# Kernel tuning notes

Hardware: AMD Instinct MI355X
Metric: run time of the kernel (lower is better)

## Reference

```python
import jax, jax.numpy as jnp
import numpy as np

B, C, H, W = 4, 256, 64, 64
C8 = C // 8


def setup_inputs() -> dict:
    key = jax.random.key(0)
    ks = jax.random.split(key, 9)
    s_in = 1.0 / np.sqrt(C)
    return {
        "x": jax.random.normal(ks[0], (B, C, H, W), dtype=jnp.float32),
        "Wq": jax.random.normal(ks[1], (C8, C), dtype=jnp.float32) * s_in,
        "bq": jax.random.normal(ks[2], (C8,), dtype=jnp.float32) * 0.01,
        "Wk": jax.random.normal(ks[3], (C8, C), dtype=jnp.float32) * s_in,
        "bk": jax.random.normal(ks[4], (C8,), dtype=jnp.float32) * 0.01,
        "Wv": jax.random.normal(ks[5], (C, C), dtype=jnp.float32) * s_in,
        "bv": jax.random.normal(ks[6], (C,), dtype=jnp.float32) * 0.01,
        "Wo": jax.random.normal(ks[7], (C, C), dtype=jnp.float32) * s_in,
        "bo": jax.random.normal(ks[8], (C,), dtype=jnp.float32) * 0.01,
    }


def reference(x, Wq, bq, Wk, bk, Wv, bv, Wo, bo):
    b, c, h, w = x.shape
    n = h * w
    xf = x.reshape(b, c, n)                                   # (B, C, N)
    # 1x1 convs are channel GEMMs
    q = jnp.einsum('bcn,dc->bnd', xf, Wq) + bq                # (B, N, C8)
    k = jnp.einsum('bcn,dc->bdn', xf, Wk) + bk[:, None]       # (B, C8, N)
    v = jnp.einsum('bcn,dc->bdn', xf, Wv) + bv[:, None]       # (B, C, N)
    energy = jnp.einsum('bnd,bdm->bnm', q, k)                 # (B, N, N)
    attn = jax.nn.softmax(energy, axis=-1)
    # out[b,c,i] = sum_j v[b,c,j] * attn[b,i,j]
    out = jnp.einsum('bcj,bij->bci', v, attn)                 # (B, C, N)
    out = out.reshape(b, c, h, w) + x                         # residual
    out = jnp.einsum('bchw,dc->bdhw', out, Wo) + bo[None, :, None, None]
    return out
```

## Files before the change

kernel.cpp:

```cpp
#include <hip/hip_runtime.h>

#define DEV __device__ __forceinline__

constexpr int B_  = 4;
constexpr int C_  = 256;
constexpr int C8_ = 32;
constexpr int N_  = 4096;
constexpr float LOG2E = 1.4426950408889634f;

using u16 = unsigned short;
using u32 = unsigned int;

typedef __attribute__((ext_vector_type(8))) short bf16x8;
typedef __attribute__((ext_vector_type(4))) float f32x4;

DEV float bf2f(u16 u) { return __uint_as_float(((u32)u) << 16); }
DEV u16   f2bf(float f) {
  u32 i = __float_as_uint(f);
  i += 0x7fffu + ((i >> 16) & 1u);
  return (u16)(i >> 16);
}
DEV u32 pack_rtz(float a, float b) {
  return __builtin_amdgcn_perm(__float_as_uint(b), __float_as_uint(a), 0x07060302);
}

DEV void lds_barrier() {
  asm volatile("s_waitcnt lgkmcnt(0)\n\ts_barrier" ::: "memory");
}

__global__ __launch_bounds__(256) void prep(
    const float* __restrict__ Wq, const float* __restrict__ Wk,
    const float* __restrict__ Wv, const float* __restrict__ Wo,
    u16* __restrict__ WqH, u16* __restrict__ WqL,
    u16* __restrict__ WkH, u16* __restrict__ WkL,
    u16* __restrict__ WvH,
    u16* __restrict__ WoH, u16* __restrict__ WoL)
{
  const int i = blockIdx.x * 256 + threadIdx.x;
  if (i < 8192) {
    float v = Wq[i] * LOG2E;
    u16 h = f2bf(v); WqH[i] = h; WqL[i] = f2bf(v - bf2f(h));
  } else if (i < 16384) {
    int off = i - 8192;
    float v = Wk[off];
    u16 h = f2bf(v); WkH[off] = h; WkL[off] = f2bf(v - bf2f(h));
  } else if (i < 81920) {
    int off = i - 16384;
    WvH[off] = f2bf(Wv[off]);
  } else {
    int off = i - 81920;
    float v = Wo[off];
    u16 h = f2bf(v); WoH[off] = h; WoL[off] = f2bf(v - bf2f(h));
  }
}

__global__ __launch_bounds__(256) void qkv_mfma(
    const float* __restrict__ x,
    const u16* __restrict__ WqH, const u16* __restrict__ WqL,
    const u16* __restrict__ WkH, const u16* __restrict__ WkL,
    const u16* __restrict__ WvH,
    const float* __restrict__ bq, const float* __restrict__ bk,
    const float* __restrict__ bv,
    u16* __restrict__ qt, u16* __restrict__ kt, u16* __restrict__ vb,
    u16* __restrict__ xTh)
{
  __shared__ float tf[32][260];
  __shared__ __align__(16) u16 xsh[32][270];
  __shared__ __align__(16) u16 xsl[32][270];

  const int tid = threadIdx.x;
  const int lane = tid & 63, w = tid >> 6, m = lane & 15, quad = lane >> 4;
  const int b = blockIdx.y, n0 = blockIdx.x * 32;

  {
    const int nl = tid & 31, ch = tid >> 5;
    #pragma unroll
    for (int cc = 0; cc < 32; ++cc) {
      int c = ch * 32 + cc;
      tf[nl][c] = x[((size_t)b * C_ + c) * N_ + n0 + nl];
    }
  }
  __syncthreads();

  {
    const int n = tid >> 3;
    const int cb = (tid & 7) * 8;
    #pragma unroll
    for (int it = 0; it < 4; ++it) {
      int c = cb + it * 64;
      u32 ph[4], pl[4];
      #pragma unroll
      for (int j = 0; j < 4; ++j) {
        float v0 = tf[n][c + 2 * j], v1 = tf[n][c + 2 * j + 1];
        u16 h0 = f2bf(v0), h1 = f2bf(v1);
        ph[j] = (u32)h0 | ((u32)h1 << 16);
        pl[j] = (u32)f2bf(v0 - bf2f(h0)) | ((u32)f2bf(v1 - bf2f(h1)) << 16);
      }
      uint4 hv = make_uint4(ph[0], ph[1], ph[2], ph[3]);
      *(uint4*)&xsh[n][c] = hv;
      *(uint4*)&xsl[n][c] = make_uint4(pl[0], pl[1], pl[2], pl[3]);
      *(uint4*)&xTh[((size_t)b * N_ + n0 + n) * C_ + c] = hv;
    }
  }
  __syncthreads();

  const u16* qkH = (w < 2) ? (WqH + (size_t)(w * 16 + m) * C_)
                           : (WkH + (size_t)((w - 2) * 16 + m) * C_);
  const u16* qkL = (w < 2) ? (WqL + (size_t)(w * 16 + m) * C_)
                           : (WkL + (size_t)((w - 2) * 16 + m) * C_);

  f32x4 ov[4][2], oq[2];
  #pragma unroll
  for (int dt = 0; dt < 4; ++dt)
    #pragma unroll
    for (int nt = 0; nt < 2; ++nt) ov[dt][nt] = (f32x4){0.f, 0.f, 0.f, 0.f};
  #pragma unroll
  for (int nt = 0; nt < 2; ++nt) oq[nt] = (f32x4){0.f, 0.f, 0.f, 0.f};

  for (int K = 0; K < 8; ++K) {
    const int ko = K * 32 + quad * 8;
    bf16x8 xh[2], xl[2];
    #pragma unroll
    for (int nt = 0; nt < 2; ++nt) {
      xh[nt] = *(const bf16x8*)&xsh[nt * 16 + m][ko];
      xl[nt] = *(const bf16x8*)&xsl[nt * 16 + m][ko];
    }
    #pragma unroll
    for (int dt = 0; dt < 4; ++dt) {
      bf16x8 whi = *(const bf16x8*)(WvH + (size_t)(64 * w + dt * 16 + m) * C_ + ko);
      #pragma unroll
      for (int nt = 0; nt < 2; ++nt)
        ov[dt][nt] = __builtin_amdgcn_mfma_f32_16x16x32_bf16(whi, xh[nt], ov[dt][nt], 0, 0, 0);
    }
    {
      bf16x8 bhi = *(const bf16x8*)(qkH + ko);
      bf16x8 blo = *(const bf16x8*)(qkL + ko);
      #pragma unroll
      for (int nt = 0; nt < 2; ++nt) {
        oq[nt] = __builtin_amdgcn_mfma_f32_16x16x32_bf16(xh[nt], bhi, oq[nt], 0, 0, 0);
        oq[nt] = __builtin_amdgcn_mfma_f32_16x16x32_bf16(xl[nt], bhi, oq[nt], 0, 0, 0);
        oq[nt] = __builtin_amdgcn_mfma_f32_16x16x32_bf16(xh[nt], blo, oq[nt], 0, 0, 0);
      }
    }
  }

  #pragma unroll
  for (int dt = 0; dt < 4; ++dt)
    #pragma unroll
    for (int r = 0; r < 4; ++r) {
      int oc = 64 * w + dt * 16 + quad * 4 + r;
      float bias = bv[oc];
      #pragma unroll
      for (int nt = 0; nt < 2; ++nt)
        vb[((size_t)b * C_ + oc) * N_ + n0 + nt * 16 + m] = f2bf(ov[dt][nt][r] + bias);
    }
  {
    u16* qk_out = (w < 2) ? qt : kt;
    int dbase = (w & 1) * 16;
    float bias = (w < 2) ? bq[dbase + m] * LOG2E : bk[dbase + m];
    #pragma unroll
    for (int nt = 0; nt < 2; ++nt)
      #pragma unroll
      for (int r = 0; r < 4; ++r)
        qk_out[((size_t)b * N_ + n0 + nt * 16 + quad * 4 + r) * C8_ + dbase + m] =
            f2bf(oq[nt][r] + bias);
  }
}

__global__ __launch_bounds__(256) void attn_mfma(
    const u16* __restrict__ qt, const u16* __restrict__ kt,
    const u16* __restrict__ vb,
    u16* __restrict__ Onorm, float* __restrict__ ml)
{
  __shared__ __align__(16) u16  ps[2][64][136];
  __shared__ __align__(16) float als[2][64];
  __shared__ float lfin[64];

  const int tid = threadIdx.x, lane = tid & 63, w = tid >> 6;
  const int m = lane & 15, quad = lane >> 4;

  const int lid = blockIdx.x + gridDim.x * (blockIdx.y + gridDim.y * blockIdx.z);
  const int grp = lid & 7, ksl = grp & 1, b = grp >> 1;
  const int i0 = (lid >> 3) * 64;

  const bf16x8 qfrag =
      *(const bf16x8*)(qt + ((size_t)b * N_ + i0 + w * 16 + m) * C8_ + quad * 8);
  const u16* kbase = kt + (size_t)b * N_ * C8_;
  const u16* vrow  = vb + ((size_t)b * C_ + w * 64 + m) * N_;

  f32x4 o[4][4];
  #pragma unroll
  for (int t = 0; t < 4; ++t)
    #pragma unroll
    for (int ct = 0; ct < 4; ++ct) o[t][ct] = (f32x4){0.f, 0.f, 0.f, 0.f};
  float m_r = -1e30f, l_r = 0.f;

  const int jbeg = ksl * 2048, jend = jbeg + 2048;
  int buf = 0;

  for (int j0 = jbeg; j0 < jend; j0 += 128, buf ^= 1) {
    f32x4 s[8];
    bf16x8 kA[4];
    #pragma unroll
    for (int t = 0; t < 4; ++t)
      kA[t] = *(const bf16x8*)(kbase + (size_t)(j0 + t * 16 + m) * C8_ + quad * 8);
    #pragma unroll
    for (int t = 0; t < 4; ++t)
      s[t] = __builtin_amdgcn_mfma_f32_16x16x32_bf16(
          kA[t], qfrag, (f32x4){0.f, 0.f, 0.f, 0.f}, 0, 0, 0);
    bf16x8 vB[4][2];
    #pragma unroll
    for (int ct = 0; ct < 4; ++ct)
      #pragma unroll
      for (int kk = 0; kk < 2; ++kk)
        vB[ct][kk] = *(const bf16x8*)(vrow + (size_t)ct * 16 * N_ + j0 + kk * 32 + quad * 8);
    #pragma unroll
    for (int t = 0; t < 4; ++t)
      kA[t] = *(const bf16x8*)(kbase + (size_t)(j0 + (t + 4) * 16 + m) * C8_ + quad * 8);
    #pragma unroll
    for (int t = 0; t < 4; ++t)
      s[t + 4] = __builtin_amdgcn_mfma_f32_16x16x32_bf16(
          kA[t], qfrag, (f32x4){0.f, 0.f, 0.f, 0.f}, 0, 0, 0);

    float mx = -1e30f;
    #pragma unroll
    for (int t = 0; t < 8; ++t)
      #pragma unroll
      for (int r = 0; r < 4; ++r) mx = fmaxf(mx, s[t][r]);
    mx = fmaxf(mx, __shfl_xor(mx, 16));
    mx = fmaxf(mx, __shfl_xor(mx, 32));
    float mn = (mx - m_r <= 8.f) ? m_r : mx;
    float al = exp2f(m_r - mn);
    m_r = mn;
    float sm = 0.f;
    #pragma unroll
    for (int t = 0; t < 8; ++t)
      #pragma unroll
      for (int r = 0; r < 4; ++r) {
        s[t][r] = exp2f(s[t][r] - mn);
        sm += s[t][r];
      }
    sm += __shfl_xor(sm, 16);
    sm += __shfl_xor(sm, 32);
    l_r = l_r * al + sm;

    #pragma unroll
    for (int t = 0; t < 8; ++t)
      *(uint2*)&ps[buf][w * 16 + m][t * 16 + quad * 4] =
          make_uint2(pack_rtz(s[t][0], s[t][1]), pack_rtz(s[t][2], s[t][3]));
    if (quad == 0) als[buf][w * 16 + m] = al;

    lds_barrier();

    #pragma unroll
    for (int t = 0; t < 4; ++t) {
      float4 alv = *(const float4*)&als[buf][t * 16 + quad * 4];
      int need = (alv.x < 1.f) | (alv.y < 1.f) | (alv.z < 1.f) | (alv.w < 1.f);
      if (__any(need)) {
        #pragma unroll
        for (int ct = 0; ct < 4; ++ct) {
          o[t][ct][0] *= alv.x; o[t][ct][1] *= alv.y;
          o[t][ct][2] *= alv.z; o[t][ct][3] *= alv.w;
        }
      }
    }

    #pragma unroll
    for (int kk = 0; kk < 2; ++kk)
      #pragma unroll
      for (int t = 0; t < 4; ++t) {
        bf16x8 pf = *(const bf16x8*)&ps[buf][t * 16 + m][kk * 32 + quad * 8];
        #pragma unroll
        for (int ct = 0; ct < 4; ++ct)
          o[t][ct] = __builtin_amdgcn_mfma_f32_16x16x32_bf16(pf, vB[ct][kk], o[t][ct], 0, 0, 0);
      }

    __builtin_amdgcn_sched_barrier(0);

    #pragma unroll
    for (int ct = 0; ct < 4; ++ct)
      #pragma unroll
      for (int kk = 0; kk < 2; ++kk)
        vB[ct][kk] = *(const bf16x8*)(vrow + (size_t)ct * 16 * N_ + j0 + (kk + 2) * 32 + quad * 8);

    #pragma unroll
    for (int kk = 0; kk < 2; ++kk)
      #pragma unroll
      for (int t = 0; t < 4; ++t) {
        bf16x8 pf = *(const bf16x8*)&ps[buf][t * 16 + m][(kk + 2) * 32 + quad * 8];
        #pragma unroll
        for (int ct = 0; ct < 4; ++ct)
          o[t][ct] = __builtin_amdgcn_mfma_f32_16x16x32_bf16(pf, vB[ct][kk], o[t][ct], 0, 0, 0);
      }
  }

  if (quad == 0) lfin[w * 16 + m] = 1.f / l_r;
  lds_barrier();

  u16* Ob = Onorm + (((size_t)ksl * B_ + b) * N_ + i0) * C_ + w * 64;
  #pragma unroll
  for (int t = 0; t < 4; ++t) {
    float4 lv = *(const float4*)&lfin[t * 16 + quad * 4];
    float linv[4] = {lv.x, lv.y, lv.z, lv.w};
    #pragma unroll
    for (int ct = 0; ct < 4; ++ct)
      #pragma unroll
      for (int r = 0; r < 4; ++r)
        Ob[(size_t)(t * 16 + quad * 4 + r) * C_ + ct * 16 + m] = f2bf(o[t][ct][r] * linv[r]);
  }

  if (quad == 0) {
    size_t mli = ((size_t)ksl * B_ + b) * N_ + i0 + w * 16 + m;
    ml[mli] = m_r;
    ml[(size_t)2 * B_ * N_ + mli] = l_r;
  }
}

__global__ __launch_bounds__(256) void out_mfma(
    const u16* __restrict__ Onorm, const float* __restrict__ ml,
    const u16* __restrict__ xTh,
    const u16* __restrict__ WoH, const u16* __restrict__ WoL,
    const float* __restrict__ bo, float* __restrict__ out)
{
  __shared__ __align__(16) u16 hs[32][270];

  const int tid = threadIdx.x;
  const int lane = tid & 63, w = tid >> 6, m = lane & 15, quad = lane >> 4;
  const int b = blockIdx.y, n0 = blockIdx.x * 32;
  constexpr size_t BN = (size_t)B_ * N_;

  #pragma unroll
  for (int it = 0; it < 4; ++it) {
    int chunk = tid + it * 256;
    int row = chunk >> 5, col = (chunk & 31) * 8;
    size_t nrow = (size_t)b * N_ + n0 + row;

    float mm0 = ml[nrow], mm1 = ml[BN + nrow];
    float M = fmaxf(mm0, mm1);
    float ws[2];
    ws[0] = ml[2 * BN + nrow] * exp2f(mm0 - M);
    ws[1] = ml[3 * BN + nrow] * exp2f(mm1 - M);
    float inv = 1.f / (ws[0] + ws[1]);
    ws[0] *= inv; ws[1] *= inv;

    uint4 xv = *(const uint4*)(xTh + nrow * C_ + col);
    u32 xq[4] = {xv.x, xv.y, xv.z, xv.w};
    float acc[8];
    #pragma unroll
    for (int j = 0; j < 4; ++j) {
      acc[2 * j]     = bf2f((u16)(xq[j] & 0xffff));
      acc[2 * j + 1] = bf2f((u16)(xq[j] >> 16));
    }
    #pragma unroll
    for (int s = 0; s < 2; ++s) {
      uint4 ovv = *(const uint4*)(Onorm + (s * BN + nrow) * C_ + col);
      u32 oq[4] = {ovv.x, ovv.y, ovv.z, ovv.w};
      #pragma unroll
      for (int j = 0; j < 4; ++j) {
        acc[2 * j]     += ws[s] * bf2f((u16)(oq[j] & 0xffff));
        acc[2 * j + 1] += ws[s] * bf2f((u16)(oq[j] >> 16));
      }
    }
    uint4 pk;
    pk.x = (u32)f2bf(acc[0]) | ((u32)f2bf(acc[1]) << 16);
    pk.y = (u32)f2bf(acc[2]) | ((u32)f2bf(acc[3]) << 16);
    pk.z = (u32)f2bf(acc[4]) | ((u32)f2bf(acc[5]) << 16);
    pk.w = (u32)f2bf(acc[6]) | ((u32)f2bf(acc[7]) << 16);
    *(uint4*)&hs[row][col] = pk;
  }
  __syncthreads();

  f32x4 o[4][2];
  #pragma unroll
  for (int dt = 0; dt < 4; ++dt)
    #pragma unroll
    for (int nt = 0; nt < 2; ++nt) o[dt][nt] = (f32x4){0.f, 0.f, 0.f, 0.f};

  for (int K = 0; K < 8; ++K) {
    const int ko = K * 32 + quad * 8;
    bf16x8 hf[2];
    #pragma unroll
    for (int nt = 0; nt < 2; ++nt) hf[nt] = *(const bf16x8*)&hs[nt * 16 + m][ko];
    #pragma unroll
    for (int dt = 0; dt < 4; ++dt) {
      bf16x8 whi = *(const bf16x8*)(WoH + (size_t)(64 * w + dt * 16 + m) * C_ + ko);
      bf16x8 wlo = *(const bf16x8*)(WoL + (size_t)(64 * w + dt * 16 + m) * C_ + ko);
      #pragma unroll
      for (int nt = 0; nt < 2; ++nt) {
        o[dt][nt] = __builtin_amdgcn_mfma_f32_16x16x32_bf16(whi, hf[nt], o[dt][nt], 0, 0, 0);
        o[dt][nt] = __builtin_amdgcn_mfma_f32_16x16x32_bf16(wlo, hf[nt], o[dt][nt], 0, 0, 0);
      }
    }
  }

  #pragma unroll
  for (int dt = 0; dt < 4; ++dt)
    #pragma unroll
    for (int r = 0; r < 4; ++r) {
      int d = 64 * w + dt * 16 + quad * 4 + r;
      float bias = bo[d];
      #pragma unroll
      for (int nt = 0; nt < 2; ++nt)
        out[((size_t)b * C_ + d) * N_ + n0 + nt * 16 + m] = o[dt][nt][r] + bias;
    }
}

extern "C" void kernel_launch(void* const* d_in, const int* in_sizes, int n_in,
                              void* d_out, int out_size, void* d_ws, size_t ws_size,
                              hipStream_t stream)
{
  const float* x  = (const float*)d_in[0];
  const float* Wq = (const float*)d_in[1];
  const float* bq = (const float*)d_in[2];
  const float* Wk = (const float*)d_in[3];
  const float* bk = (const float*)d_in[4];
  const float* Wv = (const float*)d_in[5];
  const float* bv = (const float*)d_in[6];
  const float* Wo = (const float*)d_in[7];
  const float* bo = (const float*)d_in[8];

  u16* p = (u16*)d_ws;
  u16* qt  = p;  p += (size_t)B_ * N_ * C8_;
  u16* kt  = p;  p += (size_t)B_ * N_ * C8_;
  u16* vb  = p;  p += (size_t)B_ * C_ * N_;
  u16* xTh = p;  p += (size_t)B_ * N_ * C_;
  u16* WqH = p;  p += 8192;
  u16* WqL = p;  p += 8192;
  u16* WkH = p;  p += 8192;
  u16* WkL = p;  p += 8192;
  u16* WvH = p;  p += 65536;
  u16* WoH = p;  p += 65536;
  u16* WoL = p;  p += 65536;
  float* ml = (float*)p;  p += (size_t)8 * B_ * N_;
  u16* Onorm = p;

  float* out = (float*)d_out;

  prep<<<576, 256, 0, stream>>>(Wq, Wk, Wv, Wo,
      WqH, WqL, WkH, WkL, WvH, WoH, WoL);
  qkv_mfma<<<dim3(N_ / 32, B_), 256, 0, stream>>>(
      x, WqH, WqL, WkH, WkL, WvH, bq, bk, bv, qt, kt, vb, xTh);
  attn_mfma<<<dim3(N_ / 64, 2, B_), 256, 0, stream>>>(qt, kt, vb, Onorm, ml);
  out_mfma<<<dim3(N_ / 32, B_), 256, 0, stream>>>(Onorm, ml, xTh, WoH, WoL, bo, out);
}
```

Measured before the change: 198.4 us.

## Software-pipeline attention loop: compute next tile's QK and softmax during PV MFMAs

Restructures the flash-attention main loop into a prologue plus a steady-state loop. Each iteration now issues the next tile's K loads and QK MFMAs, and does its softmax and P store into the alternate LDS buffer, around the current tile's PV MFMAs. The next tile's first V fragments are also prefetched, so the barrier moves to the end of the iteration. The aim is to overlap exp/max VALU work and global load latency with matrix-core work. The cost is higher register pressure from live s, kA and vB across the PV phase, which could reduce occupancy.

```diff
diff --git a/kernel.cpp b/kernel.cpp
--- a/kernel.cpp
+++ b/kernel.cpp
@@ -196,27 +196,26 @@
   float m_r = -1e30f, l_r = 0.f;
 
   const int jbeg = ksl * 2048, jend = jbeg + 2048;
-  int buf = 0;
-
-  for (int j0 = jbeg; j0 < jend; j0 += 128, buf ^= 1) {
+  bf16x8 vB[4][2];
+
+  {
     f32x4 s[8];
     bf16x8 kA[4];
     #pragma unroll
     for (int t = 0; t < 4; ++t)
-      kA[t] = *(const bf16x8*)(kbase + (size_t)(j0 + t * 16 + m) * C8_ + quad * 8);
+      kA[t] = *(const bf16x8*)(kbase + (size_t)(jbeg + t * 16 + m) * C8_ + quad * 8);
     #pragma unroll
     for (int t = 0; t < 4; ++t)
       s[t] = __builtin_amdgcn_mfma_f32_16x16x32_bf16(
           kA[t], qfrag, (f32x4){0.f, 0.f, 0.f, 0.f}, 0, 0, 0);
-    bf16x8 vB[4][2];
     #pragma unroll
     for (int ct = 0; ct < 4; ++ct)
       #pragma unroll
       for (int kk = 0; kk < 2; ++kk)
-        vB[ct][kk] = *(const bf16x8*)(vrow + (size_t)ct * 16 * N_ + j0 + kk * 32 + quad * 8);
+        vB[ct][kk] = *(const bf16x8*)(vrow + (size_t)ct * 16 * N_ + jbeg + kk * 32 + quad * 8);
     #pragma unroll
     for (int t = 0; t < 4; ++t)
-      kA[t] = *(const bf16x8*)(kbase + (size_t)(j0 + (t + 4) * 16 + m) * C8_ + quad * 8);
+      kA[t] = *(const bf16x8*)(kbase + (size_t)(jbeg + (t + 4) * 16 + m) * C8_ + quad * 8);
     #pragma unroll
     for (int t = 0; t < 4; ++t)
       s[t + 4] = __builtin_amdgcn_mfma_f32_16x16x32_bf16(
@@ -246,11 +245,24 @@
 
     #pragma unroll
     for (int t = 0; t < 8; ++t)
-      *(uint2*)&ps[buf][w * 16 + m][t * 16 + quad * 4] =
+      *(uint2*)&ps[0][w * 16 + m][t * 16 + quad * 4] =
           make_uint2(pack_rtz(s[t][0], s[t][1]), pack_rtz(s[t][2], s[t][3]));
-    if (quad == 0) als[buf][w * 16 + m] = al;
-
-    lds_barrier();
+    if (quad == 0) als[0][w * 16 + m] = al;
+  }
+  lds_barrier();
+
+  int buf = 0;
+  for (int j0 = jbeg; j0 < jend; j0 += 128, buf ^= 1) {
+    const int jn = j0 + 128;
+    const bool more = jn < jend;
+
+    f32x4 s[8];
+    bf16x8 kA[4];
+    if (more) {
+      #pragma unroll
+      for (int t = 0; t < 4; ++t)
+        kA[t] = *(const bf16x8*)(kbase + (size_t)(jn + t * 16 + m) * C8_ + quad * 8);
+    }
 
     #pragma unroll
     for (int t = 0; t < 4; ++t) {
@@ -265,6 +277,20 @@
       }
     }
 
+    if (more) {
+      #pragma unroll
+      for (int t = 0; t < 4; ++t)
+        s[t] = __builtin_amdgcn_mfma_f32_16x16x32_bf16(
+            kA[t], qfrag, (f32x4){0.f, 0.f, 0.f, 0.f}, 0, 0, 0);
+      #pragma unroll
+      for (int t = 0; t < 4; ++t)
+        kA[t] = *(const bf16x8*)(kbase + (size_t)(jn + (t + 4) * 16 + m) * C8_ + quad * 8);
+      #pragma unroll
+      for (int t = 0; t < 4; ++t)
+        s[t + 4] = __builtin_amdgcn_mfma_f32_16x16x32_bf16(
+            kA[t], qfrag, (f32x4){0.f, 0.f, 0.f, 0.f}, 0, 0, 0);
+    }
+
     #pragma unroll
     for (int kk = 0; kk < 2; ++kk)
       #pragma unroll
@@ -292,6 +318,46 @@
         for (int ct = 0; ct < 4; ++ct)
           o[t][ct] = __builtin_amdgcn_mfma_f32_16x16x32_bf16(pf, vB[ct][kk], o[t][ct], 0, 0, 0);
       }
+
+    __builtin_amdgcn_sched_barrier(0);
+
+    if (more) {
+      float mx = -1e30f;
+      #pragma unroll
+      for (int t = 0; t < 8; ++t)
+        #pragma unroll
+        for (int r = 0; r < 4; ++r) mx = fmaxf(mx, s[t][r]);
+      mx = fmaxf(mx, __shfl_xor(mx, 16));
+      mx = fmaxf(mx, __shfl_xor(mx, 32));
+      float mn = (mx - m_r <= 8.f) ? m_r : mx;
+      float al = exp2f(m_r - mn);
+      m_r = mn;
+      float sm = 0.f;
+      #pragma unroll
+      for (int t = 0; t < 8; ++t)
+        #pragma unroll
+        for (int r = 0; r < 4; ++r) {
+          s[t][r] = exp2f(s[t][r] - mn);
+          sm += s[t][r];
+        }
+      sm += __shfl_xor(sm, 16);
+      sm += __shfl_xor(sm, 32);
+      l_r = l_r * al + sm;
+
+      #pragma unroll
+      for (int t = 0; t < 8; ++t)
+        *(uint2*)&ps[buf ^ 1][w * 16 + m][t * 16 + quad * 4] =
+            make_uint2(pack_rtz(s[t][0], s[t][1]), pack_rtz(s[t][2], s[t][3]));
+      if (quad == 0) als[buf ^ 1][w * 16 + m] = al;
+
+      #pragma unroll
+      for (int ct = 0; ct < 4; ++ct)
+        #pragma unroll
+        for (int kk = 0; kk < 2; ++kk)
+          vB[ct][kk] = *(const bf16x8*)(vrow + (size_t)ct * 16 * N_ + jn + kk * 32 + quad * 8);
+    }
+
+    lds_barrier();
   }
 
   if (quad == 0) lfin[w * 16 + m] = 1.f / l_r;
```

Result: slower. 203.2 us (+2.4%).

## Stage K tiles in LDS via async global_load_lds and prefetch V across iterations

Applied to the files above, without the earlier changes.

K tiles for the attention loop are now loaded cooperatively into a double-buffered LDS array with global_load_lds, and the next tile is issued right after the current QK MFMAs. Each wave then reads its K fragments from LDS instead of every wave loading them from global memory. The first half of the V fragments for the next iteration is also loaded at the end of the current one, so V load latency overlaps the remaining work. The cost is 16 KB of extra LDS per block, which may reduce occupancy, plus a full vmcnt(0) wait before the barrier that can also stall on the V loads.

```diff
diff --git a/kernel.cpp b/kernel.cpp
--- a/kernel.cpp
+++ b/kernel.cpp
@@ -26,6 +26,12 @@
 
 DEV void lds_barrier() {
   asm volatile("s_waitcnt lgkmcnt(0)\n\ts_barrier" ::: "memory");
+}
+
+DEV void gload_lds16(const u16* g, u16* l) {
+  __builtin_amdgcn_global_load_lds(
+      (const __attribute__((address_space(1))) void*)g,
+      (__attribute__((address_space(3))) void*)l, 16, 0, 0);
 }
 
 __global__ __launch_bounds__(256) void prep(
@@ -173,6 +179,7 @@
     u16* __restrict__ Onorm, float* __restrict__ ml)
 {
   __shared__ __align__(16) u16  ps[2][64][136];
+  __shared__ __align__(16) u16  ks[2][4096];
   __shared__ __align__(16) float als[2][64];
   __shared__ float lfin[64];
 
@@ -196,31 +203,54 @@
   float m_r = -1e30f, l_r = 0.f;
 
   const int jbeg = ksl * 2048, jend = jbeg + 2048;
+
+  {
+    const u16* gk = kbase + (size_t)jbeg * C8_;
+    u16* ldst = &ks[0][(w * 2) * 512];
+    const u16* gsrc = gk + (w * 2) * 512 + lane * 8;
+    gload_lds16(gsrc, ldst);
+    gload_lds16(gsrc + 512, ldst + 512);
+  }
+  asm volatile("s_waitcnt vmcnt(0)" ::: "memory");
+  __builtin_amdgcn_sched_barrier(0);
+  lds_barrier();
+
+  bf16x8 vB[4][2];
+  #pragma unroll
+  for (int ct = 0; ct < 4; ++ct)
+    #pragma unroll
+    for (int kk = 0; kk < 2; ++kk)
+      vB[ct][kk] = *(const bf16x8*)(vrow + (size_t)ct * 16 * N_ + jbeg + kk * 32 + quad * 8);
+
   int buf = 0;
-
   for (int j0 = jbeg; j0 < jend; j0 += 128, buf ^= 1) {
+    const int jn = j0 + 128;
+    const bool more = jn < jend;
+
     f32x4 s[8];
     bf16x8 kA[4];
     #pragma unroll
     for (int t = 0; t < 4; ++t)
-      kA[t] = *(const bf16x8*)(kbase + (size_t)(j0 + t * 16 + m) * C8_ + quad * 8);
+      kA[t] = *(const bf16x8*)&ks[buf][(t * 16 + m) * 32 + quad * 8];
     #pragma unroll
     for (int t = 0; t < 4; ++t)
       s[t] = __builtin_amdgcn_mfma_f32_16x16x32_bf16(
           kA[t], qfrag, (f32x4){0.f, 0.f, 0.f, 0.f}, 0, 0, 0);
-    bf16x8 vB[4][2];
-    #pragma unroll
-    for (int ct = 0; ct < 4; ++ct)
-      #pragma unroll
-      for (int kk = 0; kk < 2; ++kk)
-        vB[ct][kk] = *(const bf16x8*)(vrow + (size_t)ct * 16 * N_ + j0 + kk * 32 + quad * 8);
     #pragma unroll
     for (int t = 0; t < 4; ++t)
-      kA[t] = *(const bf16x8*)(kbase + (size_t)(j0 + (t + 4) * 16 + m) * C8_ + quad * 8);
+      kA[t] = *(const bf16x8*)&ks[buf][((t + 4) * 16 + m) * 32 + quad * 8];
     #pragma unroll
     for (int t = 0; t < 4; ++t)
       s[t + 4] = __builtin_amdgcn_mfma_f32_16x16x32_bf16(
           kA[t], qfrag, (f32x4){0.f, 0.f, 0.f, 0.f}, 0, 0, 0);
+
+    if (more) {
+      const u16* gk = kbase + (size_t)jn * C8_;
+      u16* ldst = &ks[buf ^ 1][(w * 2) * 512];
+      const u16* gsrc = gk + (w * 2) * 512 + lane * 8;
+      gload_lds16(gsrc, ldst);
+      gload_lds16(gsrc + 512, ldst + 512);
+    }
 
     float mx = -1e30f;
     #pragma unroll
@@ -249,6 +279,9 @@
       *(uint2*)&ps[buf][w * 16 + m][t * 16 + quad * 4] =
           make_uint2(pack_rtz(s[t][0], s[t][1]), pack_rtz(s[t][2], s[t][3]));
     if (quad == 0) als[buf][w * 16 + m] = al;
+
+    asm volatile("s_waitcnt vmcnt(0)" ::: "memory");
+    __builtin_amdgcn_sched_barrier(0);
 
     lds_barrier();
 
@@ -292,6 +325,16 @@
         for (int ct = 0; ct < 4; ++ct)
           o[t][ct] = __builtin_amdgcn_mfma_f32_16x16x32_bf16(pf, vB[ct][kk], o[t][ct], 0, 0, 0);
       }
+
+    __builtin_amdgcn_sched_barrier(0);
+
+    if (more) {
+      #pragma unroll
+      for (int ct = 0; ct < 4; ++ct)
+        #pragma unroll
+        for (int kk = 0; kk < 2; ++kk)
+          vB[ct][kk] = *(const bf16x8*)(vrow + (size_t)ct * 16 * N_ + jn + kk * 32 + quad * 8);
+    }
   }
 
   if (quad == 0) lfin[w * 16 + m] = 1.f / l_r;
```

After: 239.6 us. +20.8%, slower.
